# Kernel tuning notes

Hardware: AMD Instinct MI355X
Metric: run time of the kernel (lower is better)

## Reference

```python
import jax, jax.numpy as jnp
import numpy as np

C, H_IMG = 1, 1024
N_PATCH = 64
L = 12          # blocks
NH = 12         # heads
D = 768         # hidden_d
DH = D // NH    # head dim
MLP = 4 * D
OUT_D = 1000
BATCH = 256
PATCH = H_IMG // N_PATCH
IN_D = C * PATCH
SEQ = N_PATCH + 1


def _pos_emb(pos, dim):
    # faithful to original: exponent uses i directly (2*i/dim), sin for even i, cos for odd i
    p = np.arange(pos, dtype=np.float64)[:, None]
    i = np.arange(dim, dtype=np.float64)[None, :]
    ang = p / np.power(10000.0, 2.0 * i / dim)
    pe = np.where((np.arange(dim)[None, :] % 2) == 0, np.sin(ang), np.cos(ang))
    return jnp.asarray(pe, dtype=jnp.float32)


def setup_inputs() -> dict:
    key = jax.random.key(0)
    ks = jax.random.split(key, 24)
    s = lambda fan: 1.0 / np.sqrt(fan)
    inp = {
        "images": jax.random.normal(ks[0], (BATCH, C, H_IMG), jnp.float32),
        "linear_w": jax.random.uniform(ks[1], (D, IN_D), jnp.float32, -s(IN_D), s(IN_D)),
        "linear_b": jax.random.uniform(ks[2], (D,), jnp.float32, -s(IN_D), s(IN_D)),
        "class_token": jax.random.uniform(ks[3], (1, D), jnp.float32),
        "pos_emb": _pos_emb(SEQ, D),
        "ln1_g": jnp.ones((L, D), jnp.float32),
        "ln1_b": jnp.zeros((L, D), jnp.float32),
        "wq": jax.random.uniform(ks[4], (L, NH, DH, DH), jnp.float32, -s(DH), s(DH)),
        "bq": jax.random.uniform(ks[5], (L, NH, DH), jnp.float32, -s(DH), s(DH)),
        "wk": jax.random.uniform(ks[6], (L, NH, DH, DH), jnp.float32, -s(DH), s(DH)),
        "bk": jax.random.uniform(ks[7], (L, NH, DH), jnp.float32, -s(DH), s(DH)),
        "wv": jax.random.uniform(ks[8], (L, NH, DH, DH), jnp.float32, -s(DH), s(DH)),
        "bv": jax.random.uniform(ks[9], (L, NH, DH), jnp.float32, -s(DH), s(DH)),
        "ln2_g": jnp.ones((L, D), jnp.float32),
        "ln2_b": jnp.zeros((L, D), jnp.float32),
        "w1": jax.random.uniform(ks[10], (L, MLP, D), jnp.float32, -s(D), s(D)),
        "b1": jax.random.uniform(ks[11], (L, MLP), jnp.float32, -s(D), s(D)),
        "w2": jax.random.uniform(ks[12], (L, D, MLP), jnp.float32, -s(MLP), s(MLP)),
        "b2": jax.random.uniform(ks[13], (L, D), jnp.float32, -s(MLP), s(MLP)),
        "head_w": jax.random.uniform(ks[14], (OUT_D, D), jnp.float32, -s(D), s(D)),
        "head_b": jax.random.uniform(ks[15], (OUT_D,), jnp.float32, -s(D), s(D)),
    }
    return inp


def _ln(x, g, b):
    m = jnp.mean(x, axis=-1, keepdims=True)
    v = jnp.var(x, axis=-1, keepdims=True)
    return (x - m) / jnp.sqrt(v + 1e-5) * g + b


def _block(x, g1, be1, wq, bq, wk, bk, wv, bv, g2, be2, w1, bb1, w2, bb2):
    B, S, _ = x.shape
    h = _ln(x, g1, be1).reshape(B, S, NH, DH)  # split heads along feature dim
    q = jnp.einsum('bshd,hed->bshe', h, wq) + bq
    k = jnp.einsum('bshd,hed->bshe', h, wk) + bk
    v = jnp.einsum('bshd,hed->bshe', h, wv) + bv
    scores = jnp.einsum('bshe,bthe->bhst', q, k) / np.sqrt(DH).astype(np.float32)
    attn = jax.nn.softmax(scores, axis=-1)
    o = jnp.einsum('bhst,bthe->bshe', attn, v).reshape(B, S, D)
    x = x + o
    h2 = _ln(x, g2, be2)
    m = jax.nn.gelu(jnp.einsum('bsd,fd->bsf', h2, w1) + bb1, approximate=False)
    m = jnp.einsum('bsf,df->bsd', m, w2) + bb2
    return x + m


def reference(images, linear_w, linear_b, class_token, pos_emb,
              ln1_g, ln1_b, wq, bq, wk, bk, wv, bv, ln2_g, ln2_b,
              w1, b1, w2, b2, head_w, head_b):
    n = images.shape[0]
    # patchify: [n, c, h] -> [n, n_patch, c*patch_size] (flatten is (c, patch) row-major)
    patches = images.reshape(n, C, N_PATCH, PATCH).transpose(0, 2, 1, 3).reshape(n, N_PATCH, IN_D)
    tokens = jnp.einsum('npi,di->npd', patches, linear_w) + linear_b
    cls = jnp.broadcast_to(class_token[None], (n, 1, D))
    x = jnp.concatenate([cls, tokens], axis=1) + pos_emb[None]
    for l in range(L):
        x = _block(x, ln1_g[l], ln1_b[l], wq[l], bq[l], wk[l], bk[l], wv[l], bv[l],
                   ln2_g[l], ln2_b[l], w1[l], b1[l], w2[l], b2[l])
    cls_out = x[:, 0]
    logits = cls_out @ head_w.T + head_b
    return jax.nn.softmax(logits, axis=-1)
```

## Files before the change

kernel.cpp:

```cpp
#include <hip/hip_runtime.h>

#define NLAYER 12
#define NHEAD  12
#define DHEAD  64
#define DMODEL 768
#define SEQL   65
#define NBATCH 256
#define MTOK   (NBATCH*SEQL)
#define MLPD   3072

typedef _Float16 f16;
typedef f16  f16x8 __attribute__((ext_vector_type(8)));
typedef f16  f16x4 __attribute__((ext_vector_type(4)));
typedef float f32x4 __attribute__((ext_vector_type(4)));

#define MFMA(a,b,c) __builtin_amdgcn_mfma_f32_16x16x32_f16(a,b,c,0,0,0)

__device__ __forceinline__ void gload16(const void* g, void* l) {
  __builtin_amdgcn_global_load_lds((const __attribute__((address_space(1))) void*)g,
                                   (__attribute__((address_space(3))) void*)l, 16, 0, 0);
}

__device__ __forceinline__ float gelu_f(float v) {
  float z = fabsf(v) * 0.70710678118654752f;
  float t = 1.f / (1.f + 0.3275911f * z);
  float p = ((((1.061405429f*t - 1.453152027f)*t + 1.421413741f)*t
              - 0.284496736f)*t + 0.254829592f)*t;
  float erfz = 1.f - p * __expf(-z*z);
  float erfv = copysignf(erfz, v);
  return 0.5f * v * (1.f + erfv);
}

__global__ __launch_bounds__(256) void cvt_f16k(const float* __restrict__ in,
                                                f16* __restrict__ out, int n) {
  long i = ((long)blockIdx.x*256 + threadIdx.x)*4;
  if (i >= n) return;
  const float4 v = *(const float4*)(in + i);
  f16x4 o = { (f16)v.x, (f16)v.y, (f16)v.z, (f16)v.w };
  *(f16x4*)(out + i) = o;
}

__global__ __launch_bounds__(256) void patch_embed(
    const float* __restrict__ images, const float* __restrict__ lw,
    const float* __restrict__ lb, const float* __restrict__ cls,
    const float* __restrict__ pe, float* __restrict__ x) {
  const int s = blockIdx.x, n = blockIdx.y, tid = threadIdx.x;
  __shared__ float p[16];
  if (s > 0 && tid < 16) p[tid] = images[(long)n*1024 + (s-1)*16 + tid];
  __syncthreads();
  float* xr = x + ((long)n*SEQL + s)*DMODEL;
  #pragma unroll
  for (int j = 0; j < 3; ++j) {
    int d = tid + j*256;
    float v;
    if (s == 0) {
      v = cls[d] + pe[d];
    } else {
      float acc = lb[d];
      #pragma unroll
      for (int i = 0; i < 16; ++i) acc += p[i]*lw[d*16+i];
      v = acc + pe[s*DMODEL + d];
    }
    xr[d] = v;
  }
}

__global__ __launch_bounds__(256) void ln_kernel(
    const float* __restrict__ x, const float* __restrict__ g,
    const float* __restrict__ b, f16* __restrict__ out) {
  const int row = blockIdx.x, tid = threadIdx.x;
  const float* xr = x + (long)row*DMODEL;
  float v0 = xr[tid], v1 = xr[tid+256], v2 = xr[tid+512];
  float s = v0+v1+v2;
  float s2 = v0*v0 + v1*v1 + v2*v2;
  #pragma unroll
  for (int o = 32; o >= 1; o >>= 1) { s += __shfl_xor(s, o); s2 += __shfl_xor(s2, o); }
  __shared__ float red[8];
  const int wave = tid>>6, lane = tid&63;
  if (lane == 0) { red[wave] = s; red[4+wave] = s2; }
  __syncthreads();
  s  = red[0]+red[1]+red[2]+red[3];
  s2 = red[4]+red[5]+red[6]+red[7];
  float mean = s * (1.f/768.f);
  float var  = s2 * (1.f/768.f) - mean*mean;
  float rstd = rsqrtf(var + 1e-5f);
  f16* orow = out + (long)row*DMODEL;
  orow[tid]     = (f16)((v0-mean)*rstd*g[tid]     + b[tid]);
  orow[tid+256] = (f16)((v1-mean)*rstd*g[tid+256] + b[tid+256]);
  orow[tid+512] = (f16)((v2-mean)*rstd*g[tid+512] + b[tid+512]);
}

__global__ __launch_bounds__(256) void attn_kernel(
    const f16* __restrict__ h, const f16* __restrict__ wq, const f16* __restrict__ wk,
    const f16* __restrict__ wv, const float* __restrict__ bq, const float* __restrict__ bk,
    const float* __restrict__ bv, float* __restrict__ x) {
  __shared__ __align__(16) f16 HsPs[80*104];
  __shared__ __align__(16) f16 Qs[80*72];
  __shared__ __align__(16) f16 Ks[80*72];
  __shared__ __align__(16) f16 Vt[64*104];
  const int hd = blockIdx.x, b = blockIdx.y;
  const int tid = threadIdx.x, wave = tid>>6, lane = tid&63;
  const int lc = lane & 15, lg = lane >> 4;
  const f16* hbase = h + ((long)b*SEQL)*DMODEL + hd*DHEAD;

  for (int c = tid; c < 80*8; c += 256) {
    int s = c >> 3, ec = (c & 7)*8;
    uint4 val = {0u,0u,0u,0u};
    if (s < SEQL) val = *(const uint4*)(hbase + (long)s*DMODEL + ec);
    *(uint4*)&HsPs[s*104 + ec] = val;
  }
  for (int c = tid; c < 64*104/8; c += 256) {
    uint4 z = {0u,0u,0u,0u};
    *(uint4*)&Vt[c*8] = z;
  }
  __syncthreads();

  for (int task = wave; task < 15; task += 4) {
    int mat = task / 5, mt = task % 5;
    const f16* W = (mat == 0 ? wq : mat == 1 ? wk : wv) + hd*DHEAD*DHEAD;
    const float* bias = (mat == 0 ? bq : mat == 1 ? bk : bv) + hd*DHEAD;
    #pragma unroll
    for (int nt = 0; nt < 4; ++nt) {
      f32x4 a = {0.f,0.f,0.f,0.f};
      #pragma unroll
      for (int kt = 0; kt < 2; ++kt) {
        f16x8 af = *(const f16x8*)&HsPs[(mt*16 + lc)*104 + kt*32 + lg*8];
        f16x8 bf = *(const f16x8*)&W[(nt*16 + lc)*DHEAD + kt*32 + lg*8];
        a = MFMA(af, bf, a);
      }
      float bb = bias[nt*16 + lc];
      #pragma unroll
      for (int r = 0; r < 4; ++r) {
        int s = mt*16 + lg*4 + r;
        int e = nt*16 + lc;
        float v = a[r] + bb;
        if (mat == 0)      Qs[s*72 + e] = (f16)v;
        else if (mat == 1) Ks[s*72 + e] = (f16)v;
        else               Vt[e*104 + s] = (f16)v;
      }
    }
  }
  __syncthreads();

  for (int mt = wave; mt < 5; mt += 4) {
    {
      uint2 z = {0u,0u};
      *(uint2*)&HsPs[(mt*16 + (lane>>2))*104 + 80 + (lane&3)*4] = z;
    }
    f32x4 sc[5];
    #pragma unroll
    for (int nt = 0; nt < 5; ++nt) {
      f32x4 a = {0.f,0.f,0.f,0.f};
      #pragma unroll
      for (int kt = 0; kt < 2; ++kt) {
        f16x8 af = *(const f16x8*)&Qs[(mt*16 + lc)*72 + kt*32 + lg*8];
        f16x8 bf = *(const f16x8*)&Ks[(nt*16 + lc)*72 + kt*32 + lg*8];
        a = MFMA(af, bf, a);
      }
      sc[nt] = a;
    }
    #pragma unroll
    for (int r = 0; r < 4; ++r) {
      float vals[5];
      #pragma unroll
      for (int nt = 0; nt < 5; ++nt) {
        float v = sc[nt][r]*0.125f;
        if (nt*16 + lc > 64) v = -1e30f;
        vals[nt] = v;
      }
      float mx = vals[0];
      #pragma unroll
      for (int nt = 1; nt < 5; ++nt) mx = fmaxf(mx, vals[nt]);
      #pragma unroll
      for (int o = 8; o >= 1; o >>= 1) mx = fmaxf(mx, __shfl_xor(mx, o, 16));
      float sum = 0.f, p[5];
      #pragma unroll
      for (int nt = 0; nt < 5; ++nt) { p[nt] = __expf(vals[nt]-mx); sum += p[nt]; }
      #pragma unroll
      for (int o = 8; o >= 1; o >>= 1) sum += __shfl_xor(sum, o, 16);
      float inv = 1.f/sum;
      int row = mt*16 + lg*4 + r;
      #pragma unroll
      for (int nt = 0; nt < 5; ++nt) HsPs[row*104 + nt*16 + lc] = (f16)(p[nt]*inv);
    }
    f32x4 oacc[4];
    #pragma unroll
    for (int nt = 0; nt < 4; ++nt) {
      f32x4 a = {0.f,0.f,0.f,0.f};
      #pragma unroll
      for (int kt = 0; kt < 3; ++kt) {
        f16x8 af = *(const f16x8*)&HsPs[(mt*16 + lc)*104 + kt*32 + lg*8];
        f16x8 bf = *(const f16x8*)&Vt[(nt*16 + lc)*104 + kt*32 + lg*8];
        a = MFMA(af, bf, a);
      }
      oacc[nt] = a;
    }
    float* xb = x + ((long)b*SEQL)*DMODEL + hd*DHEAD;
    #pragma unroll
    for (int nt = 0; nt < 4; ++nt) {
      #pragma unroll
      for (int r = 0; r < 4; ++r) {
        int s = mt*16 + lg*4 + r;
        if (s < SEQL) {
          int e = nt*16 + lc;
          xb[(long)s*DMODEL + e] += oacc[nt][r];
        }
      }
    }
  }
}

template<int ACT>
__global__ __launch_bounds__(512, 2) void gemmQ(
    const f16* __restrict__ A, const f16* __restrict__ B,
    const float* __restrict__ bias, void* __restrict__ Cout,
    int M, int N, int K) {
  __shared__ __align__(16) f16 lds[65536];
  const int tid = threadIdx.x;
  const int wid = tid >> 6, lane = tid & 63;
  const int lr = lane & 15, lg4 = lane >> 4;
  const int wr = wid >> 2, wc = wid & 3;

  const int gx = gridDim.x;
  const int nwg = gx * gridDim.y;
  const int orig = blockIdx.y * gx + blockIdx.x;
  const int q8 = nwg >> 3, r8 = nwg & 7;
  const int xcd = orig & 7, lin = orig >> 3;
  const int wgid = (xcd < r8 ? xcd*(q8+1) : r8*(q8+1) + (xcd - r8)*q8) + lin;
  const int bx = wgid % gx, by = wgid / gx;

  const long m0 = (long)by * 256, n0 = (long)bx * 256;

  f32x4 acc[8][4];
  #pragma unroll
  for (int i = 0; i < 8; ++i)
    #pragma unroll
    for (int j = 0; j < 4; ++j) acc[i][j] = (f32x4){0.f,0.f,0.f,0.f};

  const int NT = K >> 6;

  int off[4];
  #pragma unroll
  for (int i = 0; i < 4; ++i) {
    int c = tid + i*512;
    int fr = c >> 7, ks = (c >> 6) & 1, l = c & 63;
    off[i] = (fr*16 + (l & 15))*K + ks*32 + (l >> 4)*8;
  }
  const f16* Abase = A + m0*K;
  const f16* Bbase = B + n0*K;

  auto stageA = [&](const f16* Ab, int slot) {
    f16* dst = &lds[slot*32768];
    #pragma unroll
    for (int i = 0; i < 4; ++i) gload16(Ab + off[i], &dst[(tid + i*512)*8]);
  };
  auto stageB = [&](const f16* Bb, int slot) {
    f16* dst = &lds[slot*32768 + 16384];
    #pragma unroll
    for (int i = 0; i < 4; ++i) gload16(Bb + off[i], &dst[(tid + i*512)*8]);
  };

  stageA(Abase, 0); stageB(Bbase, 0);
  Abase += 64; Bbase += 64;
  asm volatile("s_waitcnt vmcnt(0)" ::: "memory");
  asm volatile("s_barrier" ::: "memory");

  const int laneoff = lane*8;
  int slot = 0;
  for (int t = 0; t < NT; ++t) {
    const f16* As = &lds[slot*32768];
    const f16* Bs = As + 16384;
    const bool pf = (t + 1) < NT;
    f16x8 bf[4][2];
    #pragma unroll
    for (int qp = 0; qp < 4; ++qp) {
      if (qp == 0) {
        #pragma unroll
        for (int nf = 0; nf < 4; ++nf)
          #pragma unroll
          for (int ks = 0; ks < 2; ++ks)
            bf[nf][ks] = *(const f16x8*)&Bs[((wc*4 + nf)*2 + ks)*512 + laneoff];
      }
      f16x8 af[2][2];
      #pragma unroll
      for (int j = 0; j < 2; ++j)
        #pragma unroll
        for (int ks = 0; ks < 2; ++ks)
          af[j][ks] = *(const f16x8*)&As[((wr*8 + qp*2 + j)*2 + ks)*512 + laneoff];
      if (pf) {
        if (qp == 0) stageA(Abase, slot ^ 1);
        else if (qp == 1) stageB(Bbase, slot ^ 1);
      }
      asm volatile("s_barrier" ::: "memory");
      __builtin_amdgcn_s_setprio(1);
      #pragma unroll
      for (int j = 0; j < 2; ++j)
        #pragma unroll
        for (int nf = 0; nf < 4; ++nf) {
          acc[qp*2+j][nf] = MFMA(af[j][0], bf[nf][0], acc[qp*2+j][nf]);
          acc[qp*2+j][nf] = MFMA(af[j][1], bf[nf][1], acc[qp*2+j][nf]);
        }
      __builtin_amdgcn_s_setprio(0);
      if (qp == 3 && pf) asm volatile("s_waitcnt vmcnt(0)" ::: "memory");
      asm volatile("s_barrier" ::: "memory");
    }
    if (pf) { Abase += 64; Bbase += 64; }
    slot ^= 1;
  }

  if (ACT == 0) {
    char* Ct = (char*)lds;
    #pragma unroll
    for (int nf = 0; nf < 4; ++nf) {
      int col = wc*64 + nf*16 + lr;
      float bv = bias[(int)n0 + col];
      #pragma unroll
      for (int mf = 0; mf < 8; ++mf) {
        #pragma unroll
        for (int r2 = 0; r2 < 4; ++r2) {
          int row = wr*128 + mf*16 + lg4*4 + r2;
          int byte = row*512 + ((col*2) ^ ((row & 15) << 4));
          *(f16*)(Ct + byte) = (f16)gelu_f(acc[mf][nf][r2] + bv);
        }
      }
    }
    __syncthreads();
    f16* Cf = (f16*)Cout;
    #pragma unroll
    for (int i = 0; i < 16; ++i) {
      int g = i*512 + tid;
      int row = g >> 5, ch = g & 31;
      int byte = row*512 + ((ch ^ (row & 15)) << 4);
      f16x8 val = *(const f16x8*)(Ct + byte);
      *(f16x8*)(Cf + (m0 + row)*(long)N + n0 + ch*8) = val;
    }
  } else {
    float* Cf = (float*)Cout;
    #pragma unroll
    for (int nf = 0; nf < 4; ++nf) {
      int col = (int)n0 + wc*64 + nf*16 + lr;
      float bv = bias[col];
      #pragma unroll
      for (int mf = 0; mf < 8; ++mf) {
        #pragma unroll
        for (int r2 = 0; r2 < 4; ++r2) {
          long row = m0 + wr*128 + mf*16 + lg4*4 + r2;
          Cf[row*(long)N + col] += acc[mf][nf][r2] + bv;
        }
      }
    }
  }
}

__global__ __launch_bounds__(256) void head_kernel(
    const float* __restrict__ x, const float* __restrict__ hw,
    const float* __restrict__ hb, float* __restrict__ out) {
  const int b = blockIdx.x, tid = threadIdx.x;
  __shared__ float cls[768];
  __shared__ float red[8];
  const float* xr = x + (long)b*SEQL*DMODEL;
  #pragma unroll
  for (int j = 0; j < 3; ++j) cls[tid + j*256] = xr[tid + j*256];
  __syncthreads();
  float lgv[4];
  #pragma unroll
  for (int j = 0; j < 4; ++j) {
    int c = tid + j*256;
    float acc = -1e30f;
    if (c < 1000) {
      const float* wr = hw + (long)c*768;
      float s_ = 0.f;
      for (int i = 0; i < 768; ++i) s_ += cls[i]*wr[i];
      acc = s_ + hb[c];
    }
    lgv[j] = acc;
  }
  const int wave = tid>>6, lane = tid&63;
  float mx = fmaxf(fmaxf(lgv[0],lgv[1]),fmaxf(lgv[2],lgv[3]));
  #pragma unroll
  for (int o = 32; o >= 1; o >>= 1) mx = fmaxf(mx, __shfl_xor(mx, o));
  if (lane == 0) red[wave] = mx;
  __syncthreads();
  mx = fmaxf(fmaxf(red[0],red[1]),fmaxf(red[2],red[3]));
  float e[4]; float sum = 0.f;
  #pragma unroll
  for (int j = 0; j < 4; ++j) {
    int c = tid + j*256;
    e[j] = (c < 1000) ? expf(lgv[j]-mx) : 0.f;
    sum += e[j];
  }
  #pragma unroll
  for (int o = 32; o >= 1; o >>= 1) sum += __shfl_xor(sum, o);
  if (lane == 0) red[4+wave] = sum;
  __syncthreads();
  sum = red[4]+red[5]+red[6]+red[7];
  float inv = 1.f/sum;
  #pragma unroll
  for (int j = 0; j < 4; ++j) {
    int c = tid + j*256;
    if (c < 1000) out[(long)b*1000 + c] = e[j]*inv;
  }
}

extern "C" void kernel_launch(void* const* d_in, const int* in_sizes, int n_in,
                              void* d_out, int out_size, void* d_ws, size_t ws_size,
                              hipStream_t stream) {
  const float* images     = (const float*)d_in[0];
  const float* linear_w   = (const float*)d_in[1];
  const float* linear_b   = (const float*)d_in[2];
  const float* class_tok  = (const float*)d_in[3];
  const float* pos_emb    = (const float*)d_in[4];
  const float* ln1_g      = (const float*)d_in[5];
  const float* ln1_b      = (const float*)d_in[6];
  const float* wq         = (const float*)d_in[7];
  const float* bq         = (const float*)d_in[8];
  const float* wk         = (const float*)d_in[9];
  const float* bk         = (const float*)d_in[10];
  const float* wv         = (const float*)d_in[11];
  const float* bv         = (const float*)d_in[12];
  const float* ln2_g      = (const float*)d_in[13];
  const float* ln2_b      = (const float*)d_in[14];
  const float* w1         = (const float*)d_in[15];
  const float* b1         = (const float*)d_in[16];
  const float* w2         = (const float*)d_in[17];
  const float* b2         = (const float*)d_in[18];
  const float* head_w     = (const float*)d_in[19];
  const float* head_b     = (const float*)d_in[20];

  char* ws = (char*)d_ws;
  float* xbuf = (float*)(ws + 0);
  f16*   hbuf = (f16*)(ws + 51118080);
  f16*   mbuf = (f16*)(ws + 76677120);
  f16*   w1all = (f16*)(ws + 178913280);
  f16*   w2all = (f16*)(ws + 235536384);
  f16*   wqbB  = (f16*)(ws + 292159488);
  f16*   wkbB  = (f16*)(ws + 293339136);
  f16*   wvbB  = (f16*)(ws + 294518784);
  f16*   w1b  = (f16*)(ws + 178913280);
  f16*   w2b  = (f16*)(ws + 183631872);
  f16*   wqbS = (f16*)(ws + 188350464);
  f16*   wkbS = (f16*)(ws + 189530112);
  f16*   wvbS = (f16*)(ws + 190709760);
  if (ws_size < 191889408ull) return;
  const bool big = ws_size >= 295698432ull;
  f16* wqb = big ? wqbB : wqbS;
  f16* wkb = big ? wkbB : wkbS;
  f16* wvb = big ? wvbB : wvbS;

  patch_embed<<<dim3(SEQL, NBATCH), 256, 0, stream>>>(images, linear_w, linear_b,
                                                      class_tok, pos_emb, xbuf);
  cvt_f16k<<<576, 256, 0, stream>>>(wq, wqb, 589824);
  cvt_f16k<<<576, 256, 0, stream>>>(wk, wkb, 589824);
  cvt_f16k<<<576, 256, 0, stream>>>(wv, wvb, 589824);
  if (big) {
    cvt_f16k<<<27648, 256, 0, stream>>>(w1, w1all, 28311552);
    cvt_f16k<<<27648, 256, 0, stream>>>(w2, w2all, 28311552);
  }

  for (int l = 0; l < NLAYER; ++l) {
    ln_kernel<<<MTOK, 256, 0, stream>>>(xbuf, ln1_g + l*768, ln1_b + l*768, hbuf);
    attn_kernel<<<dim3(NHEAD, NBATCH), 256, 0, stream>>>(
        hbuf, wqb + l*49152, wkb + l*49152, wvb + l*49152,
        bq + l*768, bk + l*768, bv + l*768, xbuf);
    ln_kernel<<<MTOK, 256, 0, stream>>>(xbuf, ln2_g + l*768, ln2_b + l*768, hbuf);
    f16* w1p = big ? (w1all + (long)l*2359296) : w1b;
    f16* w2p = big ? (w2all + (long)l*2359296) : w2b;
    if (!big) cvt_f16k<<<2304, 256, 0, stream>>>(w1 + (long)l*2359296, w1b, 2359296);
    gemmQ<0><<<dim3(MLPD/256, MTOK/256), 512, 0, stream>>>(
        hbuf, w1p, b1 + l*3072, (void*)mbuf, MTOK, MLPD, DMODEL);
    if (!big) cvt_f16k<<<2304, 256, 0, stream>>>(w2 + (long)l*2359296, w2b, 2359296);
    gemmQ<1><<<dim3(DMODEL/256, MTOK/256), 512, 0, stream>>>(
        mbuf, w2p, b2 + l*768, (void*)xbuf, MTOK, DMODEL, MLPD);
  }
  head_kernel<<<NBATCH, 256, 0, stream>>>(xbuf, head_w, head_b, (float*)d_out);
}
```

Measured before the change: 5.374 ms.

## Rework MLP GEMM pipeline, batch LayerNorm rows per wave, widen attention block

The MLP GEMM is rewritten from a double-buffered K=64 loop with quarter-phase barriers into a triple-buffered K=32 loop. It uses one barrier per step, prefetches two stages ahead and stages the GELU epilogue in two halves to fit the smaller LDS footprint. LayerNorm now handles two rows per wave with float4 loads and f16x4 stores, dropping the cross-wave shared-memory reduction and launching one-eighth as many blocks. The attention kernel moves to 5 waves so each of the 5 row tiles gets its own wave. The risks are lower occupancy from removing the min-2-blocks launch bound and more barrier overhead per unit of work with the shorter K step.

```diff
diff --git a/kernel.cpp b/kernel.cpp
--- a/kernel.cpp
+++ b/kernel.cpp
@@ -68,29 +68,40 @@
 __global__ __launch_bounds__(256) void ln_kernel(
     const float* __restrict__ x, const float* __restrict__ g,
     const float* __restrict__ b, f16* __restrict__ out) {
-  const int row = blockIdx.x, tid = threadIdx.x;
-  const float* xr = x + (long)row*DMODEL;
-  float v0 = xr[tid], v1 = xr[tid+256], v2 = xr[tid+512];
-  float s = v0+v1+v2;
-  float s2 = v0*v0 + v1*v1 + v2*v2;
-  #pragma unroll
-  for (int o = 32; o >= 1; o >>= 1) { s += __shfl_xor(s, o); s2 += __shfl_xor(s2, o); }
-  __shared__ float red[8];
-  const int wave = tid>>6, lane = tid&63;
-  if (lane == 0) { red[wave] = s; red[4+wave] = s2; }
-  __syncthreads();
-  s  = red[0]+red[1]+red[2]+red[3];
-  s2 = red[4]+red[5]+red[6]+red[7];
-  float mean = s * (1.f/768.f);
-  float var  = s2 * (1.f/768.f) - mean*mean;
-  float rstd = rsqrtf(var + 1e-5f);
-  f16* orow = out + (long)row*DMODEL;
-  orow[tid]     = (f16)((v0-mean)*rstd*g[tid]     + b[tid]);
-  orow[tid+256] = (f16)((v1-mean)*rstd*g[tid+256] + b[tid+256]);
-  orow[tid+512] = (f16)((v2-mean)*rstd*g[tid+512] + b[tid+512]);
-}
-
-__global__ __launch_bounds__(256) void attn_kernel(
+  const int tid = threadIdx.x, wave = tid >> 6, lane = tid & 63;
+  #pragma unroll
+  for (int rr = 0; rr < 2; ++rr) {
+    const long row = (long)blockIdx.x*8 + wave*2 + rr;
+    const float* xr = x + row*DMODEL;
+    float4 v[3];
+    #pragma unroll
+    for (int j = 0; j < 3; ++j) v[j] = *(const float4*)(xr + lane*4 + j*256);
+    float s = 0.f, s2 = 0.f;
+    #pragma unroll
+    for (int j = 0; j < 3; ++j) {
+      s  += v[j].x + v[j].y + v[j].z + v[j].w;
+      s2 += v[j].x*v[j].x + v[j].y*v[j].y + v[j].z*v[j].z + v[j].w*v[j].w;
+    }
+    #pragma unroll
+    for (int o = 32; o >= 1; o >>= 1) { s += __shfl_xor(s, o); s2 += __shfl_xor(s2, o); }
+    float mean = s * (1.f/768.f);
+    float var  = s2 * (1.f/768.f) - mean*mean;
+    float rstd = rsqrtf(var + 1e-5f);
+    f16* orow = out + row*DMODEL;
+    #pragma unroll
+    for (int j = 0; j < 3; ++j) {
+      const float4 gv = *(const float4*)(g + lane*4 + j*256);
+      const float4 bv = *(const float4*)(b + lane*4 + j*256);
+      f16x4 o4 = { (f16)((v[j].x-mean)*rstd*gv.x + bv.x),
+                   (f16)((v[j].y-mean)*rstd*gv.y + bv.y),
+                   (f16)((v[j].z-mean)*rstd*gv.z + bv.z),
+                   (f16)((v[j].w-mean)*rstd*gv.w + bv.w) };
+      *(f16x4*)(orow + lane*4 + j*256) = o4;
+    }
+  }
+}
+
+__global__ __launch_bounds__(320) void attn_kernel(
     const f16* __restrict__ h, const f16* __restrict__ wq, const f16* __restrict__ wk,
     const f16* __restrict__ wv, const float* __restrict__ bq, const float* __restrict__ bk,
     const float* __restrict__ bv, float* __restrict__ x) {
@@ -103,19 +114,19 @@
   const int lc = lane & 15, lg = lane >> 4;
   const f16* hbase = h + ((long)b*SEQL)*DMODEL + hd*DHEAD;
 
-  for (int c = tid; c < 80*8; c += 256) {
+  for (int c = tid; c < 80*8; c += 320) {
     int s = c >> 3, ec = (c & 7)*8;
     uint4 val = {0u,0u,0u,0u};
     if (s < SEQL) val = *(const uint4*)(hbase + (long)s*DMODEL + ec);
     *(uint4*)&HsPs[s*104 + ec] = val;
   }
-  for (int c = tid; c < 64*104/8; c += 256) {
+  for (int c = tid; c < 64*104/8; c += 320) {
     uint4 z = {0u,0u,0u,0u};
     *(uint4*)&Vt[c*8] = z;
   }
   __syncthreads();
 
-  for (int task = wave; task < 15; task += 4) {
+  for (int task = wave; task < 15; task += 5) {
     int mat = task / 5, mt = task % 5;
     const f16* W = (mat == 0 ? wq : mat == 1 ? wk : wv) + hd*DHEAD*DHEAD;
     const float* bias = (mat == 0 ? bq : mat == 1 ? bk : bv) + hd*DHEAD;
@@ -142,7 +153,7 @@
   }
   __syncthreads();
 
-  for (int mt = wave; mt < 5; mt += 4) {
+  for (int mt = wave; mt < 5; mt += 5) {
     {
       uint2 z = {0u,0u};
       *(uint2*)&HsPs[(mt*16 + (lane>>2))*104 + 80 + (lane&3)*4] = z;
@@ -211,11 +222,11 @@
 }
 
 template<int ACT>
-__global__ __launch_bounds__(512, 2) void gemmQ(
+__global__ __launch_bounds__(512) void gemm256(
     const f16* __restrict__ A, const f16* __restrict__ B,
     const float* __restrict__ bias, void* __restrict__ Cout,
     int M, int N, int K) {
-  __shared__ __align__(16) f16 lds[65536];
+  __shared__ __align__(16) f16 lds[49152];
   const int tid = threadIdx.x;
   const int wid = tid >> 6, lane = tid & 63;
   const int lr = lane & 15, lg4 = lane >> 4;
@@ -237,102 +248,80 @@
     #pragma unroll
     for (int j = 0; j < 4; ++j) acc[i][j] = (f32x4){0.f,0.f,0.f,0.f};
 
-  const int NT = K >> 6;
-
-  int off[4];
-  #pragma unroll
-  for (int i = 0; i < 4; ++i) {
-    int c = tid + i*512;
-    int fr = c >> 7, ks = (c >> 6) & 1, l = c & 63;
-    off[i] = (fr*16 + (l & 15))*K + ks*32 + (l >> 4)*8;
-  }
+  const int NT = K >> 5;
+  const long offA0 = (long)((tid >> 6)*16 + (lane & 15))*K + (lane >> 4)*8;
+  const long offA1 = offA0 + 128*(long)K;
   const f16* Abase = A + m0*K;
   const f16* Bbase = B + n0*K;
 
-  auto stageA = [&](const f16* Ab, int slot) {
-    f16* dst = &lds[slot*32768];
-    #pragma unroll
-    for (int i = 0; i < 4; ++i) gload16(Ab + off[i], &dst[(tid + i*512)*8]);
+  auto stage = [&](int t) {
+    f16* da = &lds[(t % 3)*16384];
+    f16* db = da + 8192;
+    const f16* Ap = Abase + t*32;
+    const f16* Bp = Bbase + t*32;
+    gload16(Ap + offA0, &da[tid*8]);
+    gload16(Ap + offA1, &da[(tid+512)*8]);
+    gload16(Bp + offA0, &db[tid*8]);
+    gload16(Bp + offA1, &db[(tid+512)*8]);
   };
-  auto stageB = [&](const f16* Bb, int slot) {
-    f16* dst = &lds[slot*32768 + 16384];
-    #pragma unroll
-    for (int i = 0; i < 4; ++i) gload16(Bb + off[i], &dst[(tid + i*512)*8]);
-  };
-
-  stageA(Abase, 0); stageB(Bbase, 0);
-  Abase += 64; Bbase += 64;
-  asm volatile("s_waitcnt vmcnt(0)" ::: "memory");
-  asm volatile("s_barrier" ::: "memory");
-
-  const int laneoff = lane*8;
-  int slot = 0;
+
+  stage(0); stage(1);
+
   for (int t = 0; t < NT; ++t) {
-    const f16* As = &lds[slot*32768];
-    const f16* Bs = As + 16384;
-    const bool pf = (t + 1) < NT;
-    f16x8 bf[4][2];
-    #pragma unroll
-    for (int qp = 0; qp < 4; ++qp) {
-      if (qp == 0) {
+    const f16* As = &lds[(t % 3)*16384];
+    const f16* Bs = As + 8192;
+    if (t + 1 < NT) asm volatile("s_waitcnt vmcnt(4) lgkmcnt(0)" ::: "memory");
+    else            asm volatile("s_waitcnt vmcnt(0) lgkmcnt(0)" ::: "memory");
+    asm volatile("s_barrier" ::: "memory");
+    if (t + 2 < NT) stage(t + 2);
+    f16x8 af[8], bf[4];
+    #pragma unroll
+    for (int mf = 0; mf < 8; ++mf)
+      af[mf] = *(const f16x8*)&As[(wr*8 + mf)*512 + lane*8];
+    #pragma unroll
+    for (int nf = 0; nf < 4; ++nf)
+      bf[nf] = *(const f16x8*)&Bs[(wc*4 + nf)*512 + lane*8];
+    __builtin_amdgcn_s_setprio(1);
+    #pragma unroll
+    for (int mf = 0; mf < 8; ++mf)
+      #pragma unroll
+      for (int nf = 0; nf < 4; ++nf)
+        acc[mf][nf] = MFMA(af[mf], bf[nf], acc[mf][nf]);
+    __builtin_amdgcn_s_setprio(0);
+  }
+
+  __syncthreads();
+
+  if (ACT == 0) {
+    f16* Cf = (f16*)Cout;
+    char* Ct = (char*)lds;
+    #pragma unroll
+    for (int H = 0; H < 2; ++H) {
+      #pragma unroll
+      for (int nf = 0; nf < 4; ++nf) {
+        int col = wc*64 + nf*16 + lr;
+        float bv = bias[(int)n0 + col];
         #pragma unroll
-        for (int nf = 0; nf < 4; ++nf)
+        for (int mh = 0; mh < 4; ++mh) {
           #pragma unroll
-          for (int ks = 0; ks < 2; ++ks)
-            bf[nf][ks] = *(const f16x8*)&Bs[((wc*4 + nf)*2 + ks)*512 + laneoff];
-      }
-      f16x8 af[2][2];
-      #pragma unroll
-      for (int j = 0; j < 2; ++j)
-        #pragma unroll
-        for (int ks = 0; ks < 2; ++ks)
-          af[j][ks] = *(const f16x8*)&As[((wr*8 + qp*2 + j)*2 + ks)*512 + laneoff];
-      if (pf) {
-        if (qp == 0) stageA(Abase, slot ^ 1);
-        else if (qp == 1) stageB(Bbase, slot ^ 1);
-      }
-      asm volatile("s_barrier" ::: "memory");
-      __builtin_amdgcn_s_setprio(1);
-      #pragma unroll
-      for (int j = 0; j < 2; ++j)
-        #pragma unroll
-        for (int nf = 0; nf < 4; ++nf) {
-          acc[qp*2+j][nf] = MFMA(af[j][0], bf[nf][0], acc[qp*2+j][nf]);
-          acc[qp*2+j][nf] = MFMA(af[j][1], bf[nf][1], acc[qp*2+j][nf]);
+          for (int r2 = 0; r2 < 4; ++r2) {
+            int rloc = wr*64 + mh*16 + lg4*4 + r2;
+            int byte = rloc*512 + ((col*2) ^ ((rloc & 15) << 4));
+            *(f16*)(Ct + byte) = (f16)gelu_f(acc[H*4 + mh][nf][r2] + bv);
+          }
         }
-      __builtin_amdgcn_s_setprio(0);
-      if (qp == 3 && pf) asm volatile("s_waitcnt vmcnt(0)" ::: "memory");
-      asm volatile("s_barrier" ::: "memory");
-    }
-    if (pf) { Abase += 64; Bbase += 64; }
-    slot ^= 1;
-  }
-
-  if (ACT == 0) {
-    char* Ct = (char*)lds;
-    #pragma unroll
-    for (int nf = 0; nf < 4; ++nf) {
-      int col = wc*64 + nf*16 + lr;
-      float bv = bias[(int)n0 + col];
-      #pragma unroll
-      for (int mf = 0; mf < 8; ++mf) {
-        #pragma unroll
-        for (int r2 = 0; r2 < 4; ++r2) {
-          int row = wr*128 + mf*16 + lg4*4 + r2;
-          int byte = row*512 + ((col*2) ^ ((row & 15) << 4));
-          *(f16*)(Ct + byte) = (f16)gelu_f(acc[mf][nf][r2] + bv);
-        }
-      }
-    }
-    __syncthreads();
-    f16* Cf = (f16*)Cout;
-    #pragma unroll
-    for (int i = 0; i < 16; ++i) {
-      int g = i*512 + tid;
-      int row = g >> 5, ch = g & 31;
-      int byte = row*512 + ((ch ^ (row & 15)) << 4);
-      f16x8 val = *(const f16x8*)(Ct + byte);
-      *(f16x8*)(Cf + (m0 + row)*(long)N + n0 + ch*8) = val;
+      }
+      __syncthreads();
+      #pragma unroll
+      for (int i = 0; i < 8; ++i) {
+        int g = i*512 + tid;
+        int rloc = g >> 5, ch = g & 31;
+        int byte = rloc*512 + ((ch ^ (rloc & 15)) << 4);
+        f16x8 val = *(const f16x8*)(Ct + byte);
+        long grow = m0 + (rloc >> 6)*128 + H*64 + (rloc & 63);
+        *(f16x8*)(Cf + grow*(long)N + n0 + ch*8) = val;
+      }
+      __syncthreads();
     }
   } else {
     float* Cf = (float*)Cout;
@@ -458,18 +447,18 @@
   }
 
   for (int l = 0; l < NLAYER; ++l) {
-    ln_kernel<<<MTOK, 256, 0, stream>>>(xbuf, ln1_g + l*768, ln1_b + l*768, hbuf);
-    attn_kernel<<<dim3(NHEAD, NBATCH), 256, 0, stream>>>(
+    ln_kernel<<<MTOK/8, 256, 0, stream>>>(xbuf, ln1_g + l*768, ln1_b + l*768, hbuf);
+    attn_kernel<<<dim3(NHEAD, NBATCH), 320, 0, stream>>>(
         hbuf, wqb + l*49152, wkb + l*49152, wvb + l*49152,
         bq + l*768, bk + l*768, bv + l*768, xbuf);
-    ln_kernel<<<MTOK, 256, 0, stream>>>(xbuf, ln2_g + l*768, ln2_b + l*768, hbuf);
+    ln_kernel<<<MTOK/8, 256, 0, stream>>>(xbuf, ln2_g + l*768, ln2_b + l*768, hbuf);
     f16* w1p = big ? (w1all + (long)l*2359296) : w1b;
     f16* w2p = big ? (w2all + (long)l*2359296) : w2b;
     if (!big) cvt_f16k<<<2304, 256, 0, stream>>>(w1 + (long)l*2359296, w1b, 2359296);
-    gemmQ<0><<<dim3(MLPD/256, MTOK/256), 512, 0, stream>>>(
+    gemm256<0><<<dim3(MLPD/256, MTOK/256), 512, 0, stream>>>(
         hbuf, w1p, b1 + l*3072, (void*)mbuf, MTOK, MLPD, DMODEL);
     if (!big) cvt_f16k<<<2304, 256, 0, stream>>>(w2 + (long)l*2359296, w2b, 2359296);
-    gemmQ<1><<<dim3(DMODEL/256, MTOK/256), 512, 0, stream>>>(
+    gemm256<1><<<dim3(DMODEL/256, MTOK/256), 512, 0, stream>>>(
         mbuf, w2p, b2 + l*768, (void*)xbuf, MTOK, DMODEL, MLPD);
   }
   head_kernel<<<NBATCH, 256, 0, stream>>>(xbuf, head_w, head_b, (float*)d_out);
```

Result: faster. 5.226 ms (-2.8%).
